# Optimization experiments

Hardware: AMD Instinct MI355X
Metric: run time of the kernel (lower is better)

## Reference

```python
import jax, jax.numpy as jnp
import numpy as np

N_GENES = 15135
K = int(np.ceil(0.5 * N_GENES))  # 7568, PyG TopKPooling ratio=0.5
BS, E, F_IN, H, HF, NC, L = 8, 242160, 64, 128, 512, 2, 3


def setup_inputs() -> dict:
    key = jax.random.key(0)
    ks = jax.random.split(key, 16)
    def lin(k, fin, fout):
        s = 1.0 / np.sqrt(fin)
        return jax.random.normal(k, (fin, fout), jnp.float32) * s
    x = jax.random.normal(ks[0], (BS, N_GENES, F_IN), jnp.float32)
    batch = jnp.zeros((BS,), jnp.int32)
    edge_index = jax.random.randint(ks[1], (2, E), 0, N_GENES, dtype=jnp.int32)
    CAT = L * H
    return {
        "x": x,
        "batch": batch,
        "edge_index": edge_index,
        "W1": lin(ks[2], F_IN, H), "b1": jnp.zeros((H,), jnp.float32),
        "W2": lin(ks[3], H, H),    "b2": jnp.zeros((H,), jnp.float32),
        "W3": lin(ks[4], H, H),    "b3": jnp.zeros((H,), jnp.float32),
        "topk_w": jax.random.normal(ks[5], (CAT,), jnp.float32) / np.sqrt(CAT),
        "fcW": lin(ks[6], CAT, 1), "fcb": jnp.zeros((1,), jnp.float32),
        "lin1W": lin(ks[7], K, HF), "lin1b": jnp.zeros((HF,), jnp.float32),
        "lin2W": lin(ks[8], HF, NC), "lin2b": jnp.zeros((NC,), jnp.float32),
    }


def reference(x, batch, edge_index, W1, b1, W2, b2, W3, b3,
              topk_w, fcW, fcb, lin1W, lin1b, lin2W, lin2b):
    bs = x.shape[0]
    # --- GCN normalization with self-loops (PyG GCNConv defaults) ---
    loop = jnp.arange(N_GENES, dtype=edge_index.dtype)
    src = jnp.concatenate([edge_index[0], loop])
    dst = jnp.concatenate([edge_index[1], loop])
    deg = jnp.zeros((N_GENES,), x.dtype).at[dst].add(1.0)
    dinv = jax.lax.rsqrt(deg)  # deg >= 1 due to self-loops
    norm = dinv[src] * dinv[dst]  # [E+N]

    def gcn(h, W, b):
        h = h @ W                                   # [bs, N, H]
        msg = h[:, src, :] * norm[None, :, None]    # gather + edge weight
        agg = jnp.zeros_like(h).at[:, dst, :].add(msg)  # scatter-add
        return agg + b

    h1 = jax.nn.relu(gcn(x, W1, b1))
    h2 = jax.nn.relu(gcn(h1, W2, b2))
    h3 = jax.nn.relu(gcn(h2, W3, b3))
    # mode='cat': stack on last dim then flatten -> feature order (H, layer)
    xc = jnp.stack([h1, h2, h3], -1).reshape(bs, N_GENES, -1)  # [bs, N, L*H]

    # --- TopKPooling (score = tanh(x.w/||w||), keep top ceil(0.5*N)) ---
    score = jnp.tanh((xc @ topk_w) / jnp.linalg.norm(topk_w))  # [bs, N]
    top_s, perm = jax.lax.top_k(score, K)                       # [bs, K]
    xp = jnp.take_along_axis(xc, perm[..., None], axis=1) * top_s[..., None]

    z = (xp @ fcW + fcb)[..., 0]          # [bs, K]
    h = jax.nn.relu(z @ lin1W + lin1b)    # [bs, HF]; dropout inactive (eval)
    logits = h @ lin2W + lin2b            # [bs, NC]
    return jax.nn.log_softmax(logits, axis=-1)
```

## Files before the change

kernel.cpp:

```cpp
#include <hip/hip_runtime.h>

#define N_G   15135
#define E_N   242160
#define BSZ   8
#define K_TOP 7568
#define NH    128

__global__ void zero_kernel(int* __restrict__ p, int n) {
  int i = blockIdx.x * 1024 + threadIdx.x;
  if (i < n) p[i] = 0;
}

__global__ void count_kernel(const int* __restrict__ ei, int* __restrict__ cnt) {
  int e = blockIdx.x * 256 + threadIdx.x;
  if (e < E_N) atomicAdd(&cnt[ei[E_N + e]], 1);
}

__global__ __launch_bounds__(1024) void scan_kernel(const int* __restrict__ cnt,
                                                    int* __restrict__ rowstart,
                                                    float* __restrict__ dinv,
                                                    int* __restrict__ gctr,
                                                    const float* __restrict__ topk_w,
                                                    float* __restrict__ scal) {
  __shared__ int buf[1024];
  __shared__ int base;
  int tid = threadIdx.x;
  int i = blockIdx.x * 1024 + tid;
  int v = (i < N_G) ? cnt[i] : 0;
  if (i < N_G) dinv[i] = 1.0f / sqrtf((float)(v + 1));
  buf[tid] = v;
  __syncthreads();
  for (int s = 1; s < 1024; s <<= 1) {
    int t = (tid >= s) ? buf[tid - s] : 0;
    __syncthreads();
    buf[tid] += t;
    __syncthreads();
  }
  if (tid == 1023) base = atomicAdd(gctr, buf[1023]);
  __syncthreads();
  if (i < N_G) rowstart[i] = base + buf[tid] - v;
  if (blockIdx.x == 0) {
    __shared__ float fbuf[512];
    if (tid < 512) {
      float w = (tid < 384) ? topk_w[tid] : 0.f;
      fbuf[tid] = w * w;
    }
    __syncthreads();
    for (int s = 256; s > 0; s >>= 1) {
      if (tid < s) fbuf[tid] += fbuf[tid + s];
      __syncthreads();
    }
    if (tid == 0) scal[0] = 1.0f / sqrtf(fbuf[0]);
  }
}

__global__ void fill_kernel(const int* __restrict__ ei, const int* __restrict__ rowstart,
                            const float* __restrict__ dinv, int* __restrict__ fillc,
                            int2* __restrict__ csr) {
  int e = blockIdx.x * 256 + threadIdx.x;
  if (e < E_N) {
    int s = ei[e], d = ei[E_N + e];
    int pos = rowstart[d] + atomicAdd(&fillc[d], 1);
    csr[pos] = make_int2(s, __float_as_int(dinv[s]));
  }
}

template<int CIN>
__global__ __launch_bounds__(256, 6) void mm_kernel(const float* __restrict__ A,
                                                    const float* __restrict__ W,
                                                    float* __restrict__ out, int M) {
  __shared__ float Ast[32][36];
  __shared__ float Bst[32][132];
  __shared__ float Ast2[32][68];
  int tid = threadIdx.x;
  int rb0 = blockIdx.x * 64;
  int c0 = (tid & 31) * 4;
  int r0 = (tid >> 5) * 8;
  float acc[8][4];
#pragma unroll
  for (int i = 0; i < 8; i++)
#pragma unroll
    for (int j = 0; j < 4; j++) acc[i][j] = 0.f;

  for (int k0 = 0; k0 < CIN; k0 += 32) {
    {
      int koff = (tid & 7) * 4;
      int row = tid >> 3;
#pragma unroll
      for (int p = 0; p < 2; ++p) {
        int r = row + p * 32;
        int grow = rb0 + r;
        float4 v = make_float4(0.f, 0.f, 0.f, 0.f);
        if (grow < M) v = *(const float4*)(A + (size_t)grow * CIN + k0 + koff);
        Ast2[koff + 0][r] = v.x; Ast2[koff + 1][r] = v.y;
        Ast2[koff + 2][r] = v.z; Ast2[koff + 3][r] = v.w;
      }
    }
    {
      int cc = (tid & 31) * 4;
      int kr = tid >> 5;
#pragma unroll
      for (int p = 0; p < 4; ++p) {
        int k = kr + p * 8;
        *(float4*)&Bst[k][cc] = *(const float4*)(W + (size_t)(k0 + k) * NH + cc);
      }
    }
    __syncthreads();
#pragma unroll 4
    for (int kk = 0; kk < 32; ++kk) {
      float a[8], b[4];
      *(float4*)&a[0] = *(const float4*)&Ast2[kk][r0];
      *(float4*)&a[4] = *(const float4*)&Ast2[kk][r0 + 4];
      *(float4*)&b[0] = *(const float4*)&Bst[kk][c0];
#pragma unroll
      for (int i = 0; i < 8; i++)
#pragma unroll
        for (int j = 0; j < 4; j++)
          acc[i][j] = fmaf(a[i], b[j], acc[i][j]);
    }
    __syncthreads();
  }
#pragma unroll
  for (int i = 0; i < 8; i++) {
    int row = rb0 + r0 + i;
    if (row < M)
      *(float4*)(out + (size_t)row * NH + c0) = make_float4(acc[i][0], acc[i][1], acc[i][2], acc[i][3]);
  }
  (void)Ast[0][0];
}

__global__ __launch_bounds__(256) void agg_kernel(const float* __restrict__ hw,
                                                  const int2* __restrict__ csr,
                                                  const int* __restrict__ rowstart,
                                                  const int* __restrict__ cnt,
                                                  const float* __restrict__ dinv,
                                                  const float* __restrict__ bias,
                                                  float* __restrict__ hout) {
  int b = blockIdx.x & 7;
  int chunk = blockIdx.x >> 3;
  int wave = threadIdx.x >> 6, lane = threadIdx.x & 63;
  int d = chunk * 4 + wave;
  if (d >= N_G) return;
  const float2* hwb = (const float2*)(hw + (size_t)b * N_G * NH);
  float dv = dinv[d];
  int e0 = rowstart[d];
  int n = cnt[d];
  float2 vd = hwb[(size_t)d * 64 + lane];
  float a0x = dv * vd.x, a0y = dv * vd.y;
  float a1x = 0.f, a1y = 0.f, a2x = 0.f, a2y = 0.f, a3x = 0.f, a3y = 0.f;
  for (int l0 = 0; l0 < n; l0 += 64) {
    int idx = l0 + lane;
    int2 p = make_int2(0, 0);
    if (idx < n) p = csr[e0 + idx];
    int m = n - l0; if (m > 64) m = 64;
    int l = 0;
    for (; l + 4 <= m; l += 4) {
      int   s0 = __shfl(p.x, l + 0), s1 = __shfl(p.x, l + 1);
      int   s2 = __shfl(p.x, l + 2), s3 = __shfl(p.x, l + 3);
      float w0 = __int_as_float(__shfl(p.y, l + 0));
      float w1 = __int_as_float(__shfl(p.y, l + 1));
      float w2 = __int_as_float(__shfl(p.y, l + 2));
      float w3 = __int_as_float(__shfl(p.y, l + 3));
      float2 v0 = hwb[(size_t)s0 * 64 + lane];
      float2 v1 = hwb[(size_t)s1 * 64 + lane];
      float2 v2 = hwb[(size_t)s2 * 64 + lane];
      float2 v3 = hwb[(size_t)s3 * 64 + lane];
      a0x = fmaf(w0, v0.x, a0x); a0y = fmaf(w0, v0.y, a0y);
      a1x = fmaf(w1, v1.x, a1x); a1y = fmaf(w1, v1.y, a1y);
      a2x = fmaf(w2, v2.x, a2x); a2y = fmaf(w2, v2.y, a2y);
      a3x = fmaf(w3, v3.x, a3x); a3y = fmaf(w3, v3.y, a3y);
    }
    for (; l < m; ++l) {
      int   s = __shfl(p.x, l);
      float w = __int_as_float(__shfl(p.y, l));
      float2 v = hwb[(size_t)s * 64 + lane];
      a0x = fmaf(w, v.x, a0x); a0y = fmaf(w, v.y, a0y);
    }
  }
  float sx = a0x + a1x + a2x + a3x;
  float sy = a0y + a1y + a2y + a3y;
  float2 bb = ((const float2*)bias)[lane];
  float2 r;
  r.x = fmaxf(fmaf(dv, sx, bb.x), 0.f);
  r.y = fmaxf(fmaf(dv, sy, bb.y), 0.f);
  ((float2*)hout)[((size_t)b * N_G + d) * 64 + lane] = r;
}

__global__ __launch_bounds__(256) void agg_score_kernel(const float* __restrict__ hw,
                                                        const int2* __restrict__ csr,
                                                        const int* __restrict__ rowstart,
                                                        const int* __restrict__ cnt,
                                                        const float* __restrict__ dinv,
                                                        const float* __restrict__ bias,
                                                        const float* __restrict__ h1,
                                                        const float* __restrict__ h2,
                                                        const float* __restrict__ topk_w,
                                                        const float* __restrict__ fcW,
                                                        const float* __restrict__ scal,
                                                        unsigned long long* __restrict__ keys,
                                                        float* __restrict__ score,
                                                        float* __restrict__ d2a) {
  int b = blockIdx.x & 7;
  int chunk = blockIdx.x >> 3;
  int wave = threadIdx.x >> 6, lane = threadIdx.x & 63;
  int d = chunk * 4 + wave;
  if (d >= N_G) return;
  const float2* hwb = (const float2*)(hw + (size_t)b * N_G * NH);
  float dv = dinv[d];
  int e0 = rowstart[d];
  int n = cnt[d];
  float2 vd = hwb[(size_t)d * 64 + lane];
  float a0x = dv * vd.x, a0y = dv * vd.y;
  float a1x = 0.f, a1y = 0.f, a2x = 0.f, a2y = 0.f, a3x = 0.f, a3y = 0.f;
  for (int l0 = 0; l0 < n; l0 += 64) {
    int idx = l0 + lane;
    int2 p = make_int2(0, 0);
    if (idx < n) p = csr[e0 + idx];
    int m = n - l0; if (m > 64) m = 64;
    int l = 0;
    for (; l + 4 <= m; l += 4) {
      int   s0 = __shfl(p.x, l + 0), s1 = __shfl(p.x, l + 1);
      int   s2 = __shfl(p.x, l + 2), s3 = __shfl(p.x, l + 3);
      float w0 = __int_as_float(__shfl(p.y, l + 0));
      float w1 = __int_as_float(__shfl(p.y, l + 1));
      float w2 = __int_as_float(__shfl(p.y, l + 2));
      float w3 = __int_as_float(__shfl(p.y, l + 3));
      float2 v0 = hwb[(size_t)s0 * 64 + lane];
      float2 v1 = hwb[(size_t)s1 * 64 + lane];
      float2 v2 = hwb[(size_t)s2 * 64 + lane];
      float2 v3 = hwb[(size_t)s3 * 64 + lane];
      a0x = fmaf(w0, v0.x, a0x); a0y = fmaf(w0, v0.y, a0y);
      a1x = fmaf(w1, v1.x, a1x); a1y = fmaf(w1, v1.y, a1y);
      a2x = fmaf(w2, v2.x, a2x); a2y = fmaf(w2, v2.y, a2y);
      a3x = fmaf(w3, v3.x, a3x); a3y = fmaf(w3, v3.y, a3y);
    }
    for (; l < m; ++l) {
      int   s = __shfl(p.x, l);
      float w = __int_as_float(__shfl(p.y, l));
      float2 v = hwb[(size_t)s * 64 + lane];
      a0x = fmaf(w, v.x, a0x); a0y = fmaf(w, v.y, a0y);
    }
  }
  float sx = a0x + a1x + a2x + a3x;
  float sy = a0y + a1y + a2y + a3y;
  float2 bb = ((const float2*)bias)[lane];
  float2 r;
  r.x = fmaxf(fmaf(dv, sx, bb.x), 0.f);
  r.y = fmaxf(fmaf(dv, sy, bb.y), 0.f);
  size_t rbase = ((size_t)b * N_G + d) * 64 + lane;
  float2 u1 = ((const float2*)h1)[rbase];
  float2 u2 = ((const float2*)h2)[rbase];
  const float2* tw2 = (const float2*)topk_w;
  const float2* fw2 = (const float2*)fcW;
  float2 ta = tw2[lane * 3 + 0], tb = tw2[lane * 3 + 1], tc = tw2[lane * 3 + 2];
  float2 fa = fw2[lane * 3 + 0], fb = fw2[lane * 3 + 1], fc = fw2[lane * 3 + 2];
  float d1 = u1.x * ta.x + u2.x * ta.y + r.x * tb.x
           + u1.y * tb.y + u2.y * tc.x + r.y * tc.y;
  float d2 = u1.x * fa.x + u2.x * fa.y + r.x * fb.x
           + u1.y * fb.y + u2.y * fc.x + r.y * fc.y;
#pragma unroll
  for (int s = 32; s > 0; s >>= 1) {
    d1 += __shfl_down(d1, s);
    d2 += __shfl_down(d2, s);
  }
  if (lane == 0) {
    int gw = b * N_G + d;
    float sc = tanhf(d1 * scal[0]);
    score[gw] = sc;
    d2a[gw] = d2;
    unsigned int u = __float_as_uint(sc);
    unsigned int k32 = (u & 0x80000000u) ? ~u : (u | 0x80000000u);
    keys[gw] = ((unsigned long long)k32 << 32) | (unsigned long long)(0xFFFFFFFFu - (unsigned)d);
  }
}

#define RANK_JS  32
#define RANK_JCH 473
__global__ __launch_bounds__(256) void rank_kernel(const unsigned long long* __restrict__ keys,
                                                   int* __restrict__ rank) {
  int b = blockIdx.y;
  int ib = blockIdx.x >> 5;
  int js = blockIdx.x & (RANK_JS-1);
  const unsigned long long* kb = keys + (size_t)b * N_G;
  int tid = threadIdx.x;
  int i0 = ib * 2048 + tid;
  unsigned long long ki[8];
  int cnt[8];
#pragma unroll
  for (int t = 0; t < 8; t++) {
    int i = i0 + t * 256;
    ki[t] = (i < N_G) ? kb[i] : ~0ull;
    cnt[t] = 0;
  }
  int j0 = js * RANK_JCH;
  int j1 = j0 + RANK_JCH; if (j1 > N_G) j1 = N_G;
  int j = j0;
  for (; j + 8 <= j1; j += 8) {
    unsigned long long k0 = kb[j + 0], k1 = kb[j + 1], k2 = kb[j + 2], k3 = kb[j + 3];
    unsigned long long k4 = kb[j + 4], k5 = kb[j + 5], k6 = kb[j + 6], k7 = kb[j + 7];
#pragma unroll
    for (int t = 0; t < 8; t++) {
      cnt[t] += (k0 > ki[t]); cnt[t] += (k1 > ki[t]);
      cnt[t] += (k2 > ki[t]); cnt[t] += (k3 > ki[t]);
      cnt[t] += (k4 > ki[t]); cnt[t] += (k5 > ki[t]);
      cnt[t] += (k6 > ki[t]); cnt[t] += (k7 > ki[t]);
    }
  }
  for (; j < j1; ++j) {
    unsigned long long kj = kb[j];
#pragma unroll
    for (int t = 0; t < 8; t++) cnt[t] += (kj > ki[t]) ? 1 : 0;
  }
#pragma unroll
  for (int t = 0; t < 8; t++) {
    int i = i0 + t * 256;
    if (i < N_G && cnt[t] > 0) atomicAdd(&rank[b * N_G + i], cnt[t]);
  }
}

__global__ void scat_kernel(const int* __restrict__ rank, const float* __restrict__ score,
                            const float* __restrict__ d2a, const float* __restrict__ fcb,
                            float* __restrict__ z) {
  int b = blockIdx.y;
  int i = blockIdx.x * 256 + threadIdx.x;
  if (i < N_G) {
    int r = rank[b * N_G + i];
    if (r < K_TOP) z[b * K_TOP + r] = fmaf(score[b * N_G + i], d2a[b * N_G + i], fcb[0]);
  }
}

__global__ __launch_bounds__(256) void lin1_kernel(const float* __restrict__ z,
                                                   const float* __restrict__ W,
                                                   float* __restrict__ hpre) {
  __shared__ float zb[237];
  int b = blockIdx.y, rs = blockIdx.x;
  int r0 = rs * 237;
  int rn = K_TOP - r0; if (rn > 237) rn = 237;
  for (int q = threadIdx.x; q < rn; q += 256) zb[q] = z[b * K_TOP + r0 + q];
  __syncthreads();
  int c = threadIdx.x;
  float a0 = 0.f, a1 = 0.f;
  for (int r = 0; r < rn; ++r) {
    float zz = zb[r];
    const float* wr = W + (size_t)(r0 + r) * 512;
    a0 = fmaf(zz, wr[c], a0);
    a1 = fmaf(zz, wr[c + 256], a1);
  }
  atomicAdd(&hpre[b * 512 + c], a0);
  atomicAdd(&hpre[b * 512 + c + 256], a1);
}

__global__ __launch_bounds__(128) void lin2_kernel(const float* __restrict__ hpre,
                                                   const float* __restrict__ l1b,
                                                   const float* __restrict__ W2,
                                                   const float* __restrict__ l2b,
                                                   float* __restrict__ out) {
  int b = blockIdx.x, tid = threadIdx.x;
  float a0 = 0.f, a1 = 0.f;
  for (int j = tid; j < 512; j += 128) {
    float t = fmaxf(hpre[b * 512 + j] + l1b[j], 0.f);
    a0 = fmaf(t, W2[j * 2 + 0], a0);
    a1 = fmaf(t, W2[j * 2 + 1], a1);
  }
#pragma unroll
  for (int s = 32; s > 0; s >>= 1) {
    a0 += __shfl_down(a0, s);
    a1 += __shfl_down(a1, s);
  }
  __shared__ float red[2][2];
  if ((tid & 63) == 0) { red[tid >> 6][0] = a0; red[tid >> 6][1] = a1; }
  __syncthreads();
  if (tid == 0) {
    float l0 = red[0][0] + red[1][0] + l2b[0];
    float l1 = red[0][1] + red[1][1] + l2b[1];
    float m = fmaxf(l0, l1);
    float lse = m + logf(expf(l0 - m) + expf(l1 - m));
    out[b * 2 + 0] = l0 - lse;
    out[b * 2 + 1] = l1 - lse;
  }
}

extern "C" void kernel_launch(void* const* d_in, const int* in_sizes, int n_in,
                              void* d_out, int out_size, void* d_ws, size_t ws_size,
                              hipStream_t stream) {
  const float* x   = (const float*)d_in[0];
  const int*   ei  = (const int*)d_in[2];
  const float* W1  = (const float*)d_in[3];
  const float* b1  = (const float*)d_in[4];
  const float* W2  = (const float*)d_in[5];
  const float* b2  = (const float*)d_in[6];
  const float* W3  = (const float*)d_in[7];
  const float* b3  = (const float*)d_in[8];
  const float* tkw = (const float*)d_in[9];
  const float* fcW = (const float*)d_in[10];
  const float* fcb = (const float*)d_in[11];
  const float* l1W = (const float*)d_in[12];
  const float* l1b = (const float*)d_in[13];
  const float* l2W = (const float*)d_in[14];
  const float* l2b = (const float*)d_in[15];
  float* out = (float*)d_out;

  char* ws = (char*)d_ws;
  size_t off = 0;
  auto alloc = [&](size_t bytes) {
    char* p = ws + off;
    off += (bytes + 255) & ~(size_t)255;
    return p;
  };
  int*   cnt   = (int*)alloc(15136 * 4);
  int*   fillc = (int*)alloc(15136 * 4);
  int*   gctr  = (int*)alloc(256);
  int*   rank  = (int*)alloc(121088 * 4);
  float* hpre  = (float*)alloc(4096 * 4);
  int*   rowstart = (int*)alloc(15136 * 4);
  float* dinv  = (float*)alloc(15136 * 4);
  float* scal  = (float*)alloc(64);
  float* z     = (float*)alloc((size_t)BSZ * K_TOP * 4);
  float* score = (float*)alloc(121088 * 4);
  float* d2a   = (float*)alloc(121088 * 4);
  unsigned long long* keys = (unsigned long long*)alloc(121088 * 8);
  int2*  csr   = (int2*)alloc((size_t)E_N * 8);
  float* hw = (float*)alloc((size_t)BSZ * N_G * NH * 4);
  float* h1 = (float*)alloc((size_t)BSZ * N_G * NH * 4);
  float* h2 = (float*)alloc((size_t)BSZ * N_G * NH * 4);
  (void)ws_size; (void)in_sizes; (void)n_in; (void)out_size;

  int zero_n = (int)(((char*)rowstart - (char*)cnt) / 4);
  zero_kernel<<<(zero_n + 1023) / 1024, 1024, 0, stream>>>(cnt, zero_n);
  count_kernel<<<(E_N + 255) / 256, 256, 0, stream>>>(ei, cnt);
  scan_kernel<<<(N_G + 1023) / 1024, 1024, 0, stream>>>(cnt, rowstart, dinv, gctr, tkw, scal);
  fill_kernel<<<(E_N + 255) / 256, 256, 0, stream>>>(ei, rowstart, dinv, fillc, csr);

  int M = BSZ * N_G;
  dim3 mmg((M + 63) / 64);
  int aggblocks = 8 * ((N_G + 3) / 4);

  mm_kernel<64><<<mmg, 256, 0, stream>>>(x, W1, hw, M);
  agg_kernel<<<aggblocks, 256, 0, stream>>>(hw, csr, rowstart, cnt, dinv, b1, h1);
  mm_kernel<128><<<mmg, 256, 0, stream>>>(h1, W2, hw, M);
  agg_kernel<<<aggblocks, 256, 0, stream>>>(hw, csr, rowstart, cnt, dinv, b2, h2);
  mm_kernel<128><<<mmg, 256, 0, stream>>>(h2, W3, hw, M);
  agg_score_kernel<<<aggblocks, 256, 0, stream>>>(hw, csr, rowstart, cnt, dinv, b3,
                                                  h1, h2, tkw, fcW, scal, keys, score, d2a);

  dim3 rg(8 * RANK_JS, BSZ);
  rank_kernel<<<rg, 256, 0, stream>>>(keys, rank);
  dim3 scg((N_G + 255) / 256, BSZ);
  scat_kernel<<<scg, 256, 0, stream>>>(rank, score, d2a, fcb, z);
  dim3 l1g(32, BSZ);
  lin1_kernel<<<l1g, 256, 0, stream>>>(z, l1W, hpre);
  lin2_kernel<<<BSZ, 128, 0, stream>>>(hpre, l1b, l2W, l2b, out);
}
```

Measured before the change: 696.5 us.

## Replace quadratic top-k ranking with histogram bucketing; split aggregation into column halves

The all-pairs 64-bit key comparison rank kernel is replaced by a 65536-bin histogram over the upper 16 key bits, a per-batch suffix scan, a bucket scatter, and a small in-bucket rank pass. Ties are broken by index, which matches the old key ordering. Each GCN aggregation now runs as two launches, one per 64-column half. In these launches the wave-uniform node index is read through readfirstlane and edge sources are scalar-loaded, with the edge weight gathered from dinv instead of being stored in the CSR. This removes the O(N^2) ranking cost and halves CSR storage, at the price of more launches, repeated CSR reads, and an extra combine pass for the split score dot products.

```diff
diff --git a/kernel.cpp b/kernel.cpp
--- a/kernel.cpp
+++ b/kernel.cpp
@@ -5,6 +5,8 @@
 #define BSZ   8
 #define K_TOP 7568
 #define NH    128
+#define NBIN  65536
+#define SUFS  65600
 
 __global__ void zero_kernel(int* __restrict__ p, int n) {
   int i = blockIdx.x * 1024 + threadIdx.x;
@@ -55,13 +57,12 @@
 }
 
 __global__ void fill_kernel(const int* __restrict__ ei, const int* __restrict__ rowstart,
-                            const float* __restrict__ dinv, int* __restrict__ fillc,
-                            int2* __restrict__ csr) {
+                            int* __restrict__ fillc, int* __restrict__ csr) {
   int e = blockIdx.x * 256 + threadIdx.x;
   if (e < E_N) {
     int s = ei[e], d = ei[E_N + e];
     int pos = rowstart[d] + atomicAdd(&fillc[d], 1);
-    csr[pos] = make_int2(s, __float_as_int(dinv[s]));
+    csr[pos] = s;
   }
 }
 
@@ -69,7 +70,6 @@
 __global__ __launch_bounds__(256, 6) void mm_kernel(const float* __restrict__ A,
                                                     const float* __restrict__ W,
                                                     float* __restrict__ out, int M) {
-  __shared__ float Ast[32][36];
   __shared__ float Bst[32][132];
   __shared__ float Ast2[32][68];
   int tid = threadIdx.x;
@@ -126,207 +126,203 @@
     if (row < M)
       *(float4*)(out + (size_t)row * NH + c0) = make_float4(acc[i][0], acc[i][1], acc[i][2], acc[i][3]);
   }
-  (void)Ast[0][0];
-}
-
-__global__ __launch_bounds__(256) void agg_kernel(const float* __restrict__ hw,
-                                                  const int2* __restrict__ csr,
-                                                  const int* __restrict__ rowstart,
-                                                  const int* __restrict__ cnt,
-                                                  const float* __restrict__ dinv,
-                                                  const float* __restrict__ bias,
-                                                  float* __restrict__ hout) {
+}
+
+__global__ __launch_bounds__(256) void agg_half_kernel(const float* __restrict__ hw,
+                                                       const int* __restrict__ csr,
+                                                       const int* __restrict__ rowstart,
+                                                       const int* __restrict__ cnt,
+                                                       const float* __restrict__ dinv,
+                                                       const float* __restrict__ bias,
+                                                       float* __restrict__ hout, int half) {
   int b = blockIdx.x & 7;
   int chunk = blockIdx.x >> 3;
   int wave = threadIdx.x >> 6, lane = threadIdx.x & 63;
   int d = chunk * 4 + wave;
   if (d >= N_G) return;
-  const float2* hwb = (const float2*)(hw + (size_t)b * N_G * NH);
+  d = __builtin_amdgcn_readfirstlane(d);
+  int c = (half << 6) + lane;
+  const float* hwb = hw + (size_t)b * N_G * NH;
   float dv = dinv[d];
   int e0 = rowstart[d];
   int n = cnt[d];
-  float2 vd = hwb[(size_t)d * 64 + lane];
-  float a0x = dv * vd.x, a0y = dv * vd.y;
-  float a1x = 0.f, a1y = 0.f, a2x = 0.f, a2y = 0.f, a3x = 0.f, a3y = 0.f;
-  for (int l0 = 0; l0 < n; l0 += 64) {
-    int idx = l0 + lane;
-    int2 p = make_int2(0, 0);
-    if (idx < n) p = csr[e0 + idx];
-    int m = n - l0; if (m > 64) m = 64;
-    int l = 0;
-    for (; l + 4 <= m; l += 4) {
-      int   s0 = __shfl(p.x, l + 0), s1 = __shfl(p.x, l + 1);
-      int   s2 = __shfl(p.x, l + 2), s3 = __shfl(p.x, l + 3);
-      float w0 = __int_as_float(__shfl(p.y, l + 0));
-      float w1 = __int_as_float(__shfl(p.y, l + 1));
-      float w2 = __int_as_float(__shfl(p.y, l + 2));
-      float w3 = __int_as_float(__shfl(p.y, l + 3));
-      float2 v0 = hwb[(size_t)s0 * 64 + lane];
-      float2 v1 = hwb[(size_t)s1 * 64 + lane];
-      float2 v2 = hwb[(size_t)s2 * 64 + lane];
-      float2 v3 = hwb[(size_t)s3 * 64 + lane];
-      a0x = fmaf(w0, v0.x, a0x); a0y = fmaf(w0, v0.y, a0y);
-      a1x = fmaf(w1, v1.x, a1x); a1y = fmaf(w1, v1.y, a1y);
-      a2x = fmaf(w2, v2.x, a2x); a2y = fmaf(w2, v2.y, a2y);
-      a3x = fmaf(w3, v3.x, a3x); a3y = fmaf(w3, v3.y, a3y);
-    }
-    for (; l < m; ++l) {
-      int   s = __shfl(p.x, l);
-      float w = __int_as_float(__shfl(p.y, l));
-      float2 v = hwb[(size_t)s * 64 + lane];
-      a0x = fmaf(w, v.x, a0x); a0y = fmaf(w, v.y, a0y);
-    }
-  }
-  float sx = a0x + a1x + a2x + a3x;
-  float sy = a0y + a1y + a2y + a3y;
-  float2 bb = ((const float2*)bias)[lane];
-  float2 r;
-  r.x = fmaxf(fmaf(dv, sx, bb.x), 0.f);
-  r.y = fmaxf(fmaf(dv, sy, bb.y), 0.f);
-  ((float2*)hout)[((size_t)b * N_G + d) * 64 + lane] = r;
-}
-
-__global__ __launch_bounds__(256) void agg_score_kernel(const float* __restrict__ hw,
-                                                        const int2* __restrict__ csr,
-                                                        const int* __restrict__ rowstart,
-                                                        const int* __restrict__ cnt,
-                                                        const float* __restrict__ dinv,
-                                                        const float* __restrict__ bias,
-                                                        const float* __restrict__ h1,
-                                                        const float* __restrict__ h2,
-                                                        const float* __restrict__ topk_w,
-                                                        const float* __restrict__ fcW,
-                                                        const float* __restrict__ scal,
-                                                        unsigned long long* __restrict__ keys,
-                                                        float* __restrict__ score,
-                                                        float* __restrict__ d2a) {
+  const int* ce = csr + e0;
+  float a0 = dv * hwb[(size_t)d * NH + c];
+  float a1 = 0.f, a2 = 0.f, a3 = 0.f, a4 = 0.f, a5 = 0.f, a6 = 0.f, a7 = 0.f;
+  int l = 0;
+  for (; l + 8 <= n; l += 8) {
+    int s0 = ce[l+0], s1 = ce[l+1], s2 = ce[l+2], s3 = ce[l+3];
+    int s4 = ce[l+4], s5 = ce[l+5], s6 = ce[l+6], s7 = ce[l+7];
+    float w0 = dinv[s0], w1 = dinv[s1], w2 = dinv[s2], w3 = dinv[s3];
+    float w4 = dinv[s4], w5 = dinv[s5], w6 = dinv[s6], w7 = dinv[s7];
+    float v0 = hwb[(size_t)s0 * NH + c];
+    float v1 = hwb[(size_t)s1 * NH + c];
+    float v2 = hwb[(size_t)s2 * NH + c];
+    float v3 = hwb[(size_t)s3 * NH + c];
+    float v4 = hwb[(size_t)s4 * NH + c];
+    float v5 = hwb[(size_t)s5 * NH + c];
+    float v6 = hwb[(size_t)s6 * NH + c];
+    float v7 = hwb[(size_t)s7 * NH + c];
+    a0 = fmaf(w0, v0, a0); a1 = fmaf(w1, v1, a1);
+    a2 = fmaf(w2, v2, a2); a3 = fmaf(w3, v3, a3);
+    a4 = fmaf(w4, v4, a4); a5 = fmaf(w5, v5, a5);
+    a6 = fmaf(w6, v6, a6); a7 = fmaf(w7, v7, a7);
+  }
+  for (; l < n; ++l) {
+    int s = ce[l];
+    a0 = fmaf(dinv[s], hwb[(size_t)s * NH + c], a0);
+  }
+  float s = ((a0 + a1) + (a2 + a3)) + ((a4 + a5) + (a6 + a7));
+  float r = fmaxf(fmaf(dv, s, bias[c]), 0.f);
+  hout[((size_t)b * N_G + d) * NH + c] = r;
+}
+
+__global__ __launch_bounds__(256) void agg_score_half_kernel(const float* __restrict__ hw,
+                                                             const int* __restrict__ csr,
+                                                             const int* __restrict__ rowstart,
+                                                             const int* __restrict__ cnt,
+                                                             const float* __restrict__ dinv,
+                                                             const float* __restrict__ bias,
+                                                             const float* __restrict__ h1,
+                                                             const float* __restrict__ h2,
+                                                             const float* __restrict__ topk_w,
+                                                             const float* __restrict__ fcW,
+                                                             float* __restrict__ pd1,
+                                                             float* __restrict__ pd2,
+                                                             int half) {
   int b = blockIdx.x & 7;
   int chunk = blockIdx.x >> 3;
   int wave = threadIdx.x >> 6, lane = threadIdx.x & 63;
   int d = chunk * 4 + wave;
   if (d >= N_G) return;
-  const float2* hwb = (const float2*)(hw + (size_t)b * N_G * NH);
+  d = __builtin_amdgcn_readfirstlane(d);
+  int c = (half << 6) + lane;
+  const float* hwb = hw + (size_t)b * N_G * NH;
   float dv = dinv[d];
   int e0 = rowstart[d];
   int n = cnt[d];
-  float2 vd = hwb[(size_t)d * 64 + lane];
-  float a0x = dv * vd.x, a0y = dv * vd.y;
-  float a1x = 0.f, a1y = 0.f, a2x = 0.f, a2y = 0.f, a3x = 0.f, a3y = 0.f;
-  for (int l0 = 0; l0 < n; l0 += 64) {
-    int idx = l0 + lane;
-    int2 p = make_int2(0, 0);
-    if (idx < n) p = csr[e0 + idx];
-    int m = n - l0; if (m > 64) m = 64;
-    int l = 0;
-    for (; l + 4 <= m; l += 4) {
-      int   s0 = __shfl(p.x, l + 0), s1 = __shfl(p.x, l + 1);
-      int   s2 = __shfl(p.x, l + 2), s3 = __shfl(p.x, l + 3);
-      float w0 = __int_as_float(__shfl(p.y, l + 0));
-      float w1 = __int_as_float(__shfl(p.y, l + 1));
-      float w2 = __int_as_float(__shfl(p.y, l + 2));
-      float w3 = __int_as_float(__shfl(p.y, l + 3));
-      float2 v0 = hwb[(size_t)s0 * 64 + lane];
-      float2 v1 = hwb[(size_t)s1 * 64 + lane];
-      float2 v2 = hwb[(size_t)s2 * 64 + lane];
-      float2 v3 = hwb[(size_t)s3 * 64 + lane];
-      a0x = fmaf(w0, v0.x, a0x); a0y = fmaf(w0, v0.y, a0y);
-      a1x = fmaf(w1, v1.x, a1x); a1y = fmaf(w1, v1.y, a1y);
-      a2x = fmaf(w2, v2.x, a2x); a2y = fmaf(w2, v2.y, a2y);
-      a3x = fmaf(w3, v3.x, a3x); a3y = fmaf(w3, v3.y, a3y);
-    }
-    for (; l < m; ++l) {
-      int   s = __shfl(p.x, l);
-      float w = __int_as_float(__shfl(p.y, l));
-      float2 v = hwb[(size_t)s * 64 + lane];
-      a0x = fmaf(w, v.x, a0x); a0y = fmaf(w, v.y, a0y);
-    }
-  }
-  float sx = a0x + a1x + a2x + a3x;
-  float sy = a0y + a1y + a2y + a3y;
-  float2 bb = ((const float2*)bias)[lane];
-  float2 r;
-  r.x = fmaxf(fmaf(dv, sx, bb.x), 0.f);
-  r.y = fmaxf(fmaf(dv, sy, bb.y), 0.f);
-  size_t rbase = ((size_t)b * N_G + d) * 64 + lane;
-  float2 u1 = ((const float2*)h1)[rbase];
-  float2 u2 = ((const float2*)h2)[rbase];
-  const float2* tw2 = (const float2*)topk_w;
-  const float2* fw2 = (const float2*)fcW;
-  float2 ta = tw2[lane * 3 + 0], tb = tw2[lane * 3 + 1], tc = tw2[lane * 3 + 2];
-  float2 fa = fw2[lane * 3 + 0], fb = fw2[lane * 3 + 1], fc = fw2[lane * 3 + 2];
-  float d1 = u1.x * ta.x + u2.x * ta.y + r.x * tb.x
-           + u1.y * tb.y + u2.y * tc.x + r.y * tc.y;
-  float d2 = u1.x * fa.x + u2.x * fa.y + r.x * fb.x
-           + u1.y * fb.y + u2.y * fc.x + r.y * fc.y;
-#pragma unroll
-  for (int s = 32; s > 0; s >>= 1) {
-    d1 += __shfl_down(d1, s);
-    d2 += __shfl_down(d2, s);
+  const int* ce = csr + e0;
+  float a0 = dv * hwb[(size_t)d * NH + c];
+  float a1 = 0.f, a2 = 0.f, a3 = 0.f, a4 = 0.f, a5 = 0.f, a6 = 0.f, a7 = 0.f;
+  int l = 0;
+  for (; l + 8 <= n; l += 8) {
+    int s0 = ce[l+0], s1 = ce[l+1], s2 = ce[l+2], s3 = ce[l+3];
+    int s4 = ce[l+4], s5 = ce[l+5], s6 = ce[l+6], s7 = ce[l+7];
+    float w0 = dinv[s0], w1 = dinv[s1], w2 = dinv[s2], w3 = dinv[s3];
+    float w4 = dinv[s4], w5 = dinv[s5], w6 = dinv[s6], w7 = dinv[s7];
+    float v0 = hwb[(size_t)s0 * NH + c];
+    float v1 = hwb[(size_t)s1 * NH + c];
+    float v2 = hwb[(size_t)s2 * NH + c];
+    float v3 = hwb[(size_t)s3 * NH + c];
+    float v4 = hwb[(size_t)s4 * NH + c];
+    float v5 = hwb[(size_t)s5 * NH + c];
+    float v6 = hwb[(size_t)s6 * NH + c];
+    float v7 = hwb[(size_t)s7 * NH + c];
+    a0 = fmaf(w0, v0, a0); a1 = fmaf(w1, v1, a1);
+    a2 = fmaf(w2, v2, a2); a3 = fmaf(w3, v3, a3);
+    a4 = fmaf(w4, v4, a4); a5 = fmaf(w5, v5, a5);
+    a6 = fmaf(w6, v6, a6); a7 = fmaf(w7, v7, a7);
+  }
+  for (; l < n; ++l) {
+    int s = ce[l];
+    a0 = fmaf(dinv[s], hwb[(size_t)s * NH + c], a0);
+  }
+  float s = ((a0 + a1) + (a2 + a3)) + ((a4 + a5) + (a6 + a7));
+  float r = fmaxf(fmaf(dv, s, bias[c]), 0.f);
+  size_t rbase = ((size_t)b * N_G + d) * NH + c;
+  float u1 = h1[rbase];
+  float u2 = h2[rbase];
+  float d1 = u1 * topk_w[c * 3] + u2 * topk_w[c * 3 + 1] + r * topk_w[c * 3 + 2];
+  float d2 = u1 * fcW[c * 3]    + u2 * fcW[c * 3 + 1]    + r * fcW[c * 3 + 2];
+#pragma unroll
+  for (int sh = 32; sh > 0; sh >>= 1) {
+    d1 += __shfl_down(d1, sh);
+    d2 += __shfl_down(d2, sh);
   }
   if (lane == 0) {
     int gw = b * N_G + d;
-    float sc = tanhf(d1 * scal[0]);
-    score[gw] = sc;
-    d2a[gw] = d2;
-    unsigned int u = __float_as_uint(sc);
-    unsigned int k32 = (u & 0x80000000u) ? ~u : (u | 0x80000000u);
-    keys[gw] = ((unsigned long long)k32 << 32) | (unsigned long long)(0xFFFFFFFFu - (unsigned)d);
-  }
-}
-
-#define RANK_JS  32
-#define RANK_JCH 473
-__global__ __launch_bounds__(256) void rank_kernel(const unsigned long long* __restrict__ keys,
-                                                   int* __restrict__ rank) {
-  int b = blockIdx.y;
-  int ib = blockIdx.x >> 5;
-  int js = blockIdx.x & (RANK_JS-1);
-  const unsigned long long* kb = keys + (size_t)b * N_G;
-  int tid = threadIdx.x;
-  int i0 = ib * 2048 + tid;
-  unsigned long long ki[8];
-  int cnt[8];
-#pragma unroll
-  for (int t = 0; t < 8; t++) {
-    int i = i0 + t * 256;
-    ki[t] = (i < N_G) ? kb[i] : ~0ull;
-    cnt[t] = 0;
-  }
-  int j0 = js * RANK_JCH;
-  int j1 = j0 + RANK_JCH; if (j1 > N_G) j1 = N_G;
-  int j = j0;
-  for (; j + 8 <= j1; j += 8) {
-    unsigned long long k0 = kb[j + 0], k1 = kb[j + 1], k2 = kb[j + 2], k3 = kb[j + 3];
-    unsigned long long k4 = kb[j + 4], k5 = kb[j + 5], k6 = kb[j + 6], k7 = kb[j + 7];
-#pragma unroll
-    for (int t = 0; t < 8; t++) {
-      cnt[t] += (k0 > ki[t]); cnt[t] += (k1 > ki[t]);
-      cnt[t] += (k2 > ki[t]); cnt[t] += (k3 > ki[t]);
-      cnt[t] += (k4 > ki[t]); cnt[t] += (k5 > ki[t]);
-      cnt[t] += (k6 > ki[t]); cnt[t] += (k7 > ki[t]);
-    }
-  }
-  for (; j < j1; ++j) {
-    unsigned long long kj = kb[j];
-#pragma unroll
-    for (int t = 0; t < 8; t++) cnt[t] += (kj > ki[t]) ? 1 : 0;
-  }
-#pragma unroll
-  for (int t = 0; t < 8; t++) {
-    int i = i0 + t * 256;
-    if (i < N_G && cnt[t] > 0) atomicAdd(&rank[b * N_G + i], cnt[t]);
-  }
-}
-
-__global__ void scat_kernel(const int* __restrict__ rank, const float* __restrict__ score,
-                            const float* __restrict__ d2a, const float* __restrict__ fcb,
-                            float* __restrict__ z) {
+    pd1[gw * 2 + half] = d1;
+    pd2[gw * 2 + half] = d2;
+  }
+}
+
+__global__ void combine_kernel(const float* __restrict__ pd1, const float* __restrict__ pd2,
+                               const float* __restrict__ scal, float* __restrict__ score,
+                               float* __restrict__ d2a, unsigned* __restrict__ keys,
+                               int* __restrict__ hist) {
   int b = blockIdx.y;
   int i = blockIdx.x * 256 + threadIdx.x;
-  if (i < N_G) {
-    int r = rank[b * N_G + i];
-    if (r < K_TOP) z[b * K_TOP + r] = fmaf(score[b * N_G + i], d2a[b * N_G + i], fcb[0]);
-  }
+  if (i >= N_G) return;
+  int gw = b * N_G + i;
+  float d1 = pd1[2 * gw] + pd1[2 * gw + 1];
+  float d2 = pd2[2 * gw] + pd2[2 * gw + 1];
+  float sc = tanhf(d1 * scal[0]);
+  score[gw] = sc;
+  d2a[gw] = d2;
+  unsigned u = __float_as_uint(sc);
+  unsigned k32 = (u & 0x80000000u) ? ~u : (u | 0x80000000u);
+  keys[gw] = k32;
+  atomicAdd(&hist[b * NBIN + (int)(k32 >> 16)], 1);
+}
+
+__global__ __launch_bounds__(1024) void suffix_kernel(const int* __restrict__ hist,
+                                                      int* __restrict__ suf) {
+  __shared__ int buf[1024];
+  int b = blockIdx.x;
+  const int* hb = hist + b * NBIN;
+  int* sb = suf + b * SUFS;
+  int t = threadIdx.x;
+  int base = t * 64;
+  int s = 0;
+  for (int k = 0; k < 64; ++k) s += hb[base + k];
+  buf[t] = s;
+  __syncthreads();
+  for (int off = 1; off < 1024; off <<= 1) {
+    int v = (t + off < 1024) ? buf[t + off] : 0;
+    __syncthreads();
+    buf[t] += v;
+    __syncthreads();
+  }
+  int acc = buf[t] - s;
+  if (t == 0) sb[NBIN] = 0;
+  for (int k = 63; k >= 0; --k) {
+    acc += hb[base + k];
+    sb[base + k] = acc;
+  }
+}
+
+__global__ void scatter_kernel(const unsigned* __restrict__ keys, int* __restrict__ hist,
+                               const int* __restrict__ suf, int2* __restrict__ bucket) {
+  int b = blockIdx.y;
+  int i = blockIdx.x * 256 + threadIdx.x;
+  if (i >= N_G) return;
+  unsigned k = keys[b * N_G + i];
+  int bin = (int)(k >> 16);
+  int old = atomicSub(&hist[b * NBIN + bin], 1);
+  int pos = suf[b * SUFS + bin + 1] + old - 1;
+  bucket[b * N_G + pos] = make_int2((int)k, i);
+}
+
+__global__ void rank_z_kernel(const unsigned* __restrict__ keys, const int* __restrict__ suf,
+                              const int2* __restrict__ bucket, const float* __restrict__ score,
+                              const float* __restrict__ d2a, const float* __restrict__ fcb,
+                              float* __restrict__ z) {
+  int b = blockIdx.y;
+  int i = blockIdx.x * 256 + threadIdx.x;
+  if (i >= N_G) return;
+  int gw = b * N_G + i;
+  unsigned k = keys[gw];
+  int bin = (int)(k >> 16);
+  int lo = suf[b * SUFS + bin + 1];
+  int hi = suf[b * SUFS + bin];
+  int r = lo;
+  const int2* bk = bucket + b * N_G;
+  for (int p = lo; p < hi; ++p) {
+    int2 e = bk[p];
+    unsigned kj = (unsigned)e.x;
+    r += (kj > k || (kj == k && e.y < i)) ? 1 : 0;
+  }
+  if (r < K_TOP) z[b * K_TOP + r] = fmaf(score[gw], d2a[gw], fcb[0]);
 }
 
 __global__ __launch_bounds__(256) void lin1_kernel(const float* __restrict__ z,
@@ -410,16 +406,20 @@
   int*   cnt   = (int*)alloc(15136 * 4);
   int*   fillc = (int*)alloc(15136 * 4);
   int*   gctr  = (int*)alloc(256);
-  int*   rank  = (int*)alloc(121088 * 4);
   float* hpre  = (float*)alloc(4096 * 4);
+  int*   hist  = (int*)alloc((size_t)BSZ * NBIN * 4);
   int*   rowstart = (int*)alloc(15136 * 4);
   float* dinv  = (float*)alloc(15136 * 4);
   float* scal  = (float*)alloc(64);
   float* z     = (float*)alloc((size_t)BSZ * K_TOP * 4);
   float* score = (float*)alloc(121088 * 4);
   float* d2a   = (float*)alloc(121088 * 4);
-  unsigned long long* keys = (unsigned long long*)alloc(121088 * 8);
-  int2*  csr   = (int2*)alloc((size_t)E_N * 8);
+  unsigned* keys = (unsigned*)alloc(121088 * 4);
+  int*   suf   = (int*)alloc((size_t)BSZ * SUFS * 4);
+  int2*  bucket = (int2*)alloc(121088 * 8);
+  float* pd1   = (float*)alloc(121088 * 2 * 4);
+  float* pd2   = (float*)alloc(121088 * 2 * 4);
+  int*   csr   = (int*)alloc((size_t)E_N * 4);
   float* hw = (float*)alloc((size_t)BSZ * N_G * NH * 4);
   float* h1 = (float*)alloc((size_t)BSZ * N_G * NH * 4);
   float* h2 = (float*)alloc((size_t)BSZ * N_G * NH * 4);
@@ -429,24 +429,30 @@
   zero_kernel<<<(zero_n + 1023) / 1024, 1024, 0, stream>>>(cnt, zero_n);
   count_kernel<<<(E_N + 255) / 256, 256, 0, stream>>>(ei, cnt);
   scan_kernel<<<(N_G + 1023) / 1024, 1024, 0, stream>>>(cnt, rowstart, dinv, gctr, tkw, scal);
-  fill_kernel<<<(E_N + 255) / 256, 256, 0, stream>>>(ei, rowstart, dinv, fillc, csr);
+  fill_kernel<<<(E_N + 255) / 256, 256, 0, stream>>>(ei, rowstart, fillc, csr);
 
   int M = BSZ * N_G;
   dim3 mmg((M + 63) / 64);
   int aggblocks = 8 * ((N_G + 3) / 4);
 
   mm_kernel<64><<<mmg, 256, 0, stream>>>(x, W1, hw, M);
-  agg_kernel<<<aggblocks, 256, 0, stream>>>(hw, csr, rowstart, cnt, dinv, b1, h1);
+  agg_half_kernel<<<aggblocks, 256, 0, stream>>>(hw, csr, rowstart, cnt, dinv, b1, h1, 0);
+  agg_half_kernel<<<aggblocks, 256, 0, stream>>>(hw, csr, rowstart, cnt, dinv, b1, h1, 1);
   mm_kernel<128><<<mmg, 256, 0, stream>>>(h1, W2, hw, M);
-  agg_kernel<<<aggblocks, 256, 0, stream>>>(hw, csr, rowstart, cnt, dinv, b2, h2);
+  agg_half_kernel<<<aggblocks, 256, 0, stream>>>(hw, csr, rowstart, cnt, dinv, b2, h2, 0);
+  agg_half_kernel<<<aggblocks, 256, 0, stream>>>(hw, csr, rowstart, cnt, dinv, b2, h2, 1);
   mm_kernel<128><<<mmg, 256, 0, stream>>>(h2, W3, hw, M);
-  agg_score_kernel<<<aggblocks, 256, 0, stream>>>(hw, csr, rowstart, cnt, dinv, b3,
-                                                  h1, h2, tkw, fcW, scal, keys, score, d2a);
-
-  dim3 rg(8 * RANK_JS, BSZ);
-  rank_kernel<<<rg, 256, 0, stream>>>(keys, rank);
-  dim3 scg((N_G + 255) / 256, BSZ);
-  scat_kernel<<<scg, 256, 0, stream>>>(rank, score, d2a, fcb, z);
+  agg_score_half_kernel<<<aggblocks, 256, 0, stream>>>(hw, csr, rowstart, cnt, dinv, b3,
+                                                       h1, h2, tkw, fcW, pd1, pd2, 0);
+  agg_score_half_kernel<<<aggblocks, 256, 0, stream>>>(hw, csr, rowstart, cnt, dinv, b3,
+                                                       h1, h2, tkw, fcW, pd1, pd2, 1);
+
+  dim3 ng((N_G + 255) / 256, BSZ);
+  combine_kernel<<<ng, 256, 0, stream>>>(pd1, pd2, scal, score, d2a, keys, hist);
+  suffix_kernel<<<BSZ, 1024, 0, stream>>>(hist, suf);
+  scatter_kernel<<<ng, 256, 0, stream>>>(keys, hist, suf, bucket);
+  rank_z_kernel<<<ng, 256, 0, stream>>>(keys, suf, bucket, score, d2a, fcb, z);
+
   dim3 l1g(32, BSZ);
   lin1_kernel<<<l1g, 256, 0, stream>>>(z, l1W, hpre);
   lin2_kernel<<<BSZ, 128, 0, stream>>>(hpre, l1b, l2W, l2b, out);
```

Result: slower. 756.6 us (+8.6%).
